# Optimization experiments

Hardware: AMD Instinct MI355X
Metric: run time of the kernel (lower is better)

The kernel has to match this reference:

```python
import jax, jax.numpy as jnp
import numpy as np

SEQ, D, H, DH = 118, 128, 4, 32
NEG = -1e9


def _rope_tables():
    # matches the second (overwriting) computation in __init__: base=10000, dim=128
    ch = jnp.arange(0, D, 2, dtype=jnp.float32)
    inv_freq = 1.0 / (10000.0 ** (ch / D))
    t = jnp.arange(SEQ, dtype=jnp.float32)
    freqs = jnp.outer(t, inv_freq)                      # (118, 64)
    return jnp.cos(freqs).astype(jnp.bfloat16), jnp.sin(freqs).astype(jnp.bfloat16)


def _apply_rope(x, cos, sin):
    # x: (b, 118, 128); cos/sin: (118, 64) bf16 -> promote to f32 in the mul
    d = x.shape[-1] // 2
    x1, x2 = x[..., :d], x[..., d:]
    y1 = x1 * cos + x2 * sin
    y2 = -x1 * sin + x2 * cos
    return jnp.concatenate([y1, y2], axis=-1).astype(x.dtype)


def _layernorm(x, g, b, eps=1e-5):
    mu = jnp.mean(x, -1, keepdims=True)
    var = jnp.mean(jnp.square(x - mu), -1, keepdims=True)
    return (x - mu) * jax.lax.rsqrt(var + eps) * g + b


def _attention_block(x, qkv_w, qkv_b, fc2_w, fc2_b, cos, sin, mask):
    b = x.shape[0]
    qkv = x @ qkv_w.T + qkv_b                           # (b, 118, 384)
    q, k, v = jnp.split(qkv, 3, axis=-1)
    q = _apply_rope(q, cos, sin)
    k = _apply_rope(k, cos, sin)
    # faithful to view(b,118,32,4) + rearrange 'b l d h -> b h l d'
    to_heads = lambda t: jnp.transpose(t.reshape(b, SEQ, DH, H), (0, 3, 1, 2))
    q, k, v = to_heads(q), to_heads(k), to_heads(v)     # (b, 4, 118, 32)
    scores = jnp.einsum('bhqd,bhkd->bhqk', q, k) / jnp.sqrt(jnp.float32(DH))
    scores = jnp.where(mask, scores, NEG)
    attn = jax.nn.softmax(scores, axis=-1)
    y = jnp.einsum('bhqk,bhkd->bhqd', attn, v)          # (b, 4, 118, 32)
    y = jnp.transpose(y, (0, 2, 1, 3)).reshape(b, SEQ, D)
    return jax.nn.silu(y @ fc2_w.T + fc2_b)


def setup_inputs() -> dict:
    key = jax.random.key(0)
    ks = jax.random.split(key, 10)
    s = lambda fan_in: 1.0 / np.sqrt(fan_in)
    inp = {
        'x': jax.random.normal(ks[0], (8192, SEQ), jnp.float32),
        'fc1_w': jax.random.uniform(ks[1], (D, 1), jnp.float32, -1.0, 1.0),
        'fc1_b': jax.random.uniform(ks[2], (D,), jnp.float32, -1.0, 1.0),
        'qkv_w': jax.random.uniform(ks[3], (3 * D, D), jnp.float32, -s(D), s(D)),
        'qkv_b': jax.random.uniform(ks[4], (3 * D,), jnp.float32, -s(D), s(D)),
        'fc2_w': jax.random.uniform(ks[5], (D, D), jnp.float32, -s(D), s(D)),
        'fc2_b': jax.random.uniform(ks[6], (D,), jnp.float32, -s(D), s(D)),
        'fc3_w': jax.random.uniform(ks[7], (1, D), jnp.float32, -s(D), s(D)),
        'fc3_b': jax.random.uniform(ks[8], (1,), jnp.float32, -s(D), s(D)),
        'ln_g': jnp.ones((D,), jnp.float32),
        'ln_b': jnp.zeros((D,), jnp.float32),
    }
    return inp


def reference(x, fc1_w, fc1_b, qkv_w, qkv_b, fc2_w, fc2_b, fc3_w, fc3_b, ln_g, ln_b):
    cos, sin = _rope_tables()
    mask = jnp.tril(jnp.ones((SEQ, SEQ), dtype=bool))
    h = jax.nn.silu(x[..., None] @ fc1_w.T + fc1_b)     # (b, 118, 128)
    x1 = _attention_block(h, qkv_w, qkv_b, fc2_w, fc2_b, cos, sin, mask)
    x2 = x1 + _attention_block(_layernorm(x1, ln_g, ln_b), qkv_w, qkv_b, fc2_w, fc2_b, cos, sin, mask)
    return (x2 @ fc3_w.T + fc3_b).squeeze(-1)           # (b, 118)
```

## Files before the change

### kernel.cpp

```cpp
#include <hip/hip_runtime.h>
#include <hip/hip_bf16.h>

#define SEQ 118
#define YS  136
#define SQS 40
#define SVS 136

typedef __attribute__((ext_vector_type(8))) short short8;
typedef __attribute__((ext_vector_type(4))) float f32x4;

__device__ __forceinline__ f32x4 mfma16(short8 a, short8 b, f32x4 c){
  return __builtin_amdgcn_mfma_f32_16x16x32_bf16(a, b, c, 0, 0, 0);
}
__device__ __forceinline__ float bfr(float x){
  return __bfloat162float(__float2bfloat16(x));
}
__device__ __forceinline__ float rcpf(float x){ return __builtin_amdgcn_rcpf(x); }
__device__ __forceinline__ float fsilu(float z){
  return z * rcpf(1.f + exp2f(-1.442695041f * z));
}
__device__ __forceinline__ float rsum16(float v){
  v += __shfl_xor(v,1); v += __shfl_xor(v,2); v += __shfl_xor(v,4); v += __shfl_xor(v,8);
  return v;
}
__device__ __forceinline__ float rmax16(float v){
  v = fmaxf(v, __shfl_xor(v,1)); v = fmaxf(v, __shfl_xor(v,2));
  v = fmaxf(v, __shfl_xor(v,4)); v = fmaxf(v, __shfl_xor(v,8));
  return v;
}
__device__ __forceinline__ unsigned pack_bf2(float lo, float hi){
  __hip_bfloat162 h2 = __float22bfloat162_rn(float2{lo, hi});
  unsigned u; __builtin_memcpy(&u, &h2, 4);
  return u;
}
__device__ __forceinline__ float bf_lo(unsigned u){
  unsigned v = u << 16; float f; __builtin_memcpy(&f, &v, 4); return f;
}
__device__ __forceinline__ float bf_hi(unsigned u){
  unsigned v = u & 0xffff0000u; float f; __builtin_memcpy(&f, &v, 4); return f;
}

__global__ void prep_kernel(const float* __restrict__ qkv_w,
                            const float* __restrict__ fc2_w,
                            __hip_bfloat16* __restrict__ wbf,
                            unsigned* __restrict__ trig){
  int i = blockIdx.x * 256 + threadIdx.x;
  if (i < 65536){
    int seg = i >> 14;
    int r   = i & 16383;
    int row = r >> 7;
    int k   = r & 127;
    float v;
    if (seg < 3){
      int h = row >> 5, n = row & 31;
      v = qkv_w[(seg*128 + 4*n + h)*128 + k];
    } else {
      int h = k >> 5, rr = k & 31;
      int dh = (rr >> 1) + (rr & 1)*16;
      v = fc2_w[row*128 + h*32 + dh];
    }
    wbf[i] = __float2bfloat16(v);
  } else {
    int ti = i - 65536;
    int h  = ti >> 11;
    int s  = (ti >> 4) & 127;
    int cc = ti & 15;
    float invf = exp2f((float)(4*cc + h) * (-0.20762050593045f));
    float ang  = (float)s * invf;
    trig[ti] = pack_bf2(__cosf(ang), __sinf(ang));
  }
}

template<bool TABLE>
__global__ void
__attribute__((amdgpu_flat_work_group_size(512, 512), amdgpu_waves_per_eu(4, 4)))
fused_kernel(const float* __restrict__ x,
             const float* __restrict__ fc1_w, const float* __restrict__ fc1_b,
             const float* __restrict__ qkv_b,
             const float* __restrict__ fc2_b, const float* __restrict__ fc3_w,
             const float* __restrict__ fc3_b,
             const float* __restrict__ ln_g,  const float* __restrict__ ln_b,
             const __hip_bfloat16* __restrict__ wbf,
             const unsigned* __restrict__ trig,
             float* __restrict__ out)
{
  __shared__ __align__(16) char smem[64864];
  __hip_bfloat16* Ybuf = (__hip_bfloat16*)(smem);
  __hip_bfloat16* sQP  = (__hip_bfloat16*)(smem + 32096);
  __hip_bfloat16* sK   = (__hip_bfloat16*)(smem + 42336);
  __hip_bfloat16* sVt  = (__hip_bfloat16*)(smem + 52576);
  float*          sCb  = (float*)        (smem + 61280);
  float*          sQb  = (float*)        (smem + 63328);

  const __hip_bfloat16* wq  = wbf;
  const __hip_bfloat16* wk  = wbf + 16384;
  const __hip_bfloat16* wvw = wbf + 32768;
  const __hip_bfloat16* w2  = wbf + 49152;

  const int b    = blockIdx.x;
  const int tid  = threadIdx.x;
  const int wv   = tid >> 6;
  const int lane = tid & 63;
  const int c    = lane & 15;
  const int quad = lane >> 4;
  const int arow = wv*16 + c;

  {
    int i = tid;
    if (i < 512){
      float v;
      if      (i < 128) v = fc2_b[i];
      else if (i < 256) v = fc3_w[i-128];
      else if (i < 384) v = ln_g [i-256];
      else              v = ln_b [i-384];
      sCb[i] = v;
    }
    if (i < 384) sQb[i] = qkv_b[i];
  }
  __syncthreads();

  float o1[4];

  #pragma unroll 1
  for (int p = 0; p < 2; ++p){
    short8 afr[4];
    if (p == 0){
      float xs = (arow < SEQ) ? x[b*SEQ + arow] : 0.f;
      #pragma unroll
      for (int k4 = 0; k4 < 4; k4++){
        int d0 = k4*32 + quad*8;
        short8 fr;
        #pragma unroll
        for (int i = 0; i < 8; i++){
          float z = xs * fc1_w[d0+i] + fc1_b[d0+i];
          float v = fsilu(z);
          if (arow >= SEQ) v = 0.f;
          fr[i] = (short)__builtin_bit_cast(unsigned short, __float2bfloat16(v));
        }
        afr[k4] = fr;
      }
    } else {
      #pragma unroll
      for (int k4 = 0; k4 < 4; k4++){
        short8 fr = *(const short8*)(Ybuf + arow*YS + k4*32 + quad*8);
        if (arow >= SEQ) fr = (short8){0,0,0,0,0,0,0,0};
        afr[k4] = fr;
      }
    }

    #pragma unroll 1
    for (int h = 0; h < 4; ++h){
      {
        unsigned tj[4];
        float invf;
        if (TABLE){
          const unsigned* tp = trig + h*2048 + (wv*16 + quad*4)*16 + c;
          tj[0] = tp[0]; tj[1] = tp[16]; tj[2] = tp[32]; tj[3] = tp[48];
        } else {
          invf = exp2f((float)(4*c + h) * (-0.20762050593045f));
        }
        const __hip_bfloat16* wpq = wq + (h*32 + c)*128 + quad*8;
        const __hip_bfloat16* wpk = wk + (h*32 + c)*128 + quad*8;
        f32x4 q0={0,0,0,0}, q1={0,0,0,0}, k0={0,0,0,0}, k1={0,0,0,0};
        #pragma unroll
        for (int k4 = 0; k4 < 4; k4++){
          short8 bq0 = *(const short8*)(wpq + k4*32);
          short8 bq1 = *(const short8*)(wpq + 2048 + k4*32);
          short8 bk0 = *(const short8*)(wpk + k4*32);
          short8 bk1 = *(const short8*)(wpk + 2048 + k4*32);
          q0 = mfma16(afr[k4], bq0, q0);
          q1 = mfma16(afr[k4], bq1, q1);
          k0 = mfma16(afr[k4], bk0, k0);
          k1 = mfma16(afr[k4], bk1, k1);
        }
        const float KSC = 0.25500526963f;
        float bQ0 = sQb[      4*c + h], bQ1 = sQb[ 64 + 4*c + h];
        float bK0 = sQb[128 + 4*c + h], bK1 = sQb[192 + 4*c + h];
        #pragma unroll
        for (int j = 0; j < 4; j++){
          int s = wv*16 + quad*4 + j;
          float cv, sv;
          if (TABLE){
            cv = bf_lo(tj[j]); sv = bf_hi(tj[j]);
          } else {
            float ang = (float)s * invf;
            cv = bfr(__cosf(ang)); sv = bfr(__sinf(ang));
          }
          float cvq = cv*KSC, svq = sv*KSC;
          float xq1 = q0[j] + bQ0, xq2 = q1[j] + bQ1;
          float xk1 = k0[j] + bK0, xk2 = k1[j] + bK1;
          *(unsigned*)(sQP + s*SQS + 2*c) = pack_bf2( xq1*cvq + xq2*svq, -xq1*svq + xq2*cvq);
          *(unsigned*)(sK  + s*SQS + 2*c) = pack_bf2( xk1*cv  + xk2*sv , -xk1*sv  + xk2*cv );
        }
      }
      {
        const __hip_bfloat16* wpv = wvw + (h*32 + c)*128 + quad*8;
        f32x4 v0={0,0,0,0}, v1={0,0,0,0};
        #pragma unroll
        for (int k4 = 0; k4 < 4; k4++){
          short8 b0 = *(const short8*)(wpv + k4*32);
          short8 b1 = *(const short8*)(wpv + 2048 + k4*32);
          v0 = mfma16(afr[k4], b0, v0);
          v1 = mfma16(afr[k4], b1, v1);
        }
        float bV0 = sQb[256 + 4*c + h], bV1 = sQb[320 + 4*c + h];
        int s0 = wv*16 + quad*4;
        *(unsigned*)(sVt + (c   )*SVS + s0    ) = pack_bf2(v0[0]+bV0, v0[1]+bV0);
        *(unsigned*)(sVt + (c   )*SVS + s0 + 2) = pack_bf2(v0[2]+bV0, v0[3]+bV0);
        *(unsigned*)(sVt + (c+16)*SVS + s0    ) = pack_bf2(v1[0]+bV1, v1[1]+bV1);
        *(unsigned*)(sVt + (c+16)*SVS + s0 + 2) = pack_bf2(v1[2]+bV1, v1[3]+bV1);
      }
      __syncthreads();

      short8 aq = *(const short8*)(sQP + arow*SQS + quad*8);
      f32x4 sc[8];
      #pragma unroll
      for (int t = 0; t < 8; t++){
        sc[t] = (f32x4){0.f,0.f,0.f,0.f};
        if (t <= wv){
          short8 bk = *(const short8*)(sK + (t*16 + c)*SQS + quad*8);
          f32x4 z = {0,0,0,0};
          sc[t] = mfma16(aq, bk, z);
        }
      }
      float rnorm[4];
      #pragma unroll
      for (int j = 0; j < 4; j++){
        float mx = -3.0e38f;
        #pragma unroll
        for (int t = 0; t < 8; t++){
          if (t < wv){
            mx = fmaxf(mx, sc[t][j]);
          } else if (t == wv){
            float v = (c <= quad*4 + j) ? sc[t][j] : -1.0e9f;
            sc[t][j] = v;
            mx = fmaxf(mx, v);
          }
        }
        mx = rmax16(mx);
        float sum = 0.f;
        #pragma unroll
        for (int t = 0; t < 8; t++) if (t <= wv){
          float e = exp2f(sc[t][j] - mx); sc[t][j] = e; sum += e;
        }
        sum = rsum16(sum);
        rnorm[j] = rcpf(sum);
      }

      f32x4 y0 = {0,0,0,0}, y1 = {0,0,0,0};
      auto pv_quarter = [&](int qt, f32x4 pa, f32x4 pb){
        int s0 = wv*16 + quad*4;
        #pragma unroll
        for (int j = 0; j < 4; j++){
          sQP[(s0+j)*SQS + c     ] = __float2bfloat16(pa[j]);
          sQP[(s0+j)*SQS + 16 + c] = __float2bfloat16(pb[j]);
        }
        short8 ap  = *(const short8*)(sQP + arow*SQS + quad*8);
        short8 bv0 = *(const short8*)(sVt + (c   )*SVS + qt*32 + quad*8);
        short8 bv1 = *(const short8*)(sVt + (c+16)*SVS + qt*32 + quad*8);
        y0 = mfma16(ap, bv0, y0);
        y1 = mfma16(ap, bv1, y1);
      };
      int qmax = wv >> 1;
      pv_quarter(0, sc[0], sc[1]);
      if (qmax >= 1) pv_quarter(1, sc[2], sc[3]);
      if (qmax >= 2) pv_quarter(2, sc[4], sc[5]);
      if (qmax >= 3) pv_quarter(3, sc[6], sc[7]);
      #pragma unroll
      for (int j = 0; j < 4; j++){ y0[j] *= rnorm[j]; y1[j] *= rnorm[j]; }

      {
        int s0 = wv*16 + quad*4;
        #pragma unroll
        for (int j = 0; j < 4; j++)
          if (s0 + j < SEQ)
            *(unsigned*)(Ybuf + (s0+j)*YS + h*32 + 2*c) = pack_bf2(y0[j], y1[j]);
      }
      __syncthreads();
    }

    short8 ay[4];
    #pragma unroll
    for (int k4 = 0; k4 < 4; k4++)
      ay[k4] = *(const short8*)(Ybuf + arow*YS + k4*32 + quad*8);
    f32x4 xx[8];
    f32x4 S1 = {0,0,0,0}, S2 = {0,0,0,0}, S3 = {0,0,0,0};
    #pragma unroll 1
    for (int t = 0; t < 8; t++){
      f32x4 acc = {0,0,0,0};
      #pragma unroll
      for (int k4 = 0; k4 < 4; k4++){
        short8 bw = *(const short8*)(w2 + (t*16 + c)*128 + k4*32 + quad*8);
        acc = mfma16(ay[k4], bw, acc);
      }
      float bias = sCb[t*16 + c];
      float w3   = sCb[128 + t*16 + c];
      #pragma unroll
      for (int j = 0; j < 4; j++){
        float v = fsilu(acc[j] + bias);
        xx[t][j] = v;
        S1[j] += v; S2[j] += v*v; S3[j] += v*w3;
      }
    }
    #pragma unroll
    for (int j = 0; j < 4; j++){
      float s1 = rsum16(S1[j]), s2 = rsum16(S2[j]), s3 = rsum16(S3[j]);
      int s = wv*16 + quad*4 + j;
      if (p == 0){
        float mu  = s1 * (1.f/128.f);
        float var = fmaxf(s2 * (1.f/128.f) - mu*mu, 0.f);
        float rs  = rsqrtf(var + 1e-5f);
        if (s < SEQ){
          #pragma unroll
          for (int t = 0; t < 8; t++){
            int d = t*16 + c;
            Ybuf[s*YS + d] = __float2bfloat16((xx[t][j] - mu)*rs*sCb[256+d] + sCb[384+d]);
          }
        }
        o1[j] = s3;
      } else {
        if (c == 0 && s < SEQ) out[b*SEQ + s] = o1[j] + s3 + fc3_b[0];
      }
    }
    if (p == 0) __syncthreads();
  }
}

extern "C" void kernel_launch(void* const* d_in, const int* in_sizes, int n_in,
                              void* d_out, int out_size, void* d_ws, size_t ws_size,
                              hipStream_t stream){
  const float* x     = (const float*)d_in[0];
  const float* fc1_w = (const float*)d_in[1];
  const float* fc1_b = (const float*)d_in[2];
  const float* qkv_w = (const float*)d_in[3];
  const float* qkv_b = (const float*)d_in[4];
  const float* fc2_w = (const float*)d_in[5];
  const float* fc2_b = (const float*)d_in[6];
  const float* fc3_w = (const float*)d_in[7];
  const float* fc3_b = (const float*)d_in[8];
  const float* ln_g  = (const float*)d_in[9];
  const float* ln_b  = (const float*)d_in[10];

  __hip_bfloat16* wbf  = (__hip_bfloat16*)d_ws;
  unsigned*       trig = (unsigned*)((char*)d_ws + 131072);
  const bool ut = ws_size >= 131072 + 32768;

  prep_kernel<<<ut ? 288 : 256, 256, 0, stream>>>(qkv_w, fc2_w, wbf, trig);

  const int B = in_sizes[0] / SEQ;
  if (ut)
    fused_kernel<true ><<<B, 512, 0, stream>>>(x, fc1_w, fc1_b, qkv_b, fc2_b, fc3_w,
                                               fc3_b, ln_g, ln_b, wbf, trig, (float*)d_out);
  else
    fused_kernel<false><<<B, 512, 0, stream>>>(x, fc1_w, fc1_b, qkv_b, fc2_b, fc3_w,
                                               fc3_b, ln_g, ln_b, wbf, trig, (float*)d_out);
}
```

Baseline: 2.321 ms.

## Transpose QK^T MFMA and pass softmax probabilities to PV via shuffles

Swaps the MFMA operands for the score computation so each lane holds one query row's scores across the key dimension. Row max and sum then reduce mostly in registers with only two cross-lane shuffles instead of four per row. The bf16-packed probabilities are redistributed into the PV MFMA A-operand layout with lane shuffles, replacing the write to shared memory and read-back. This adds more shuffle instructions and register pressure in exchange for less LDS traffic and fewer reductions.

New measurement: 2.428 ms. 4.6% more time.

```diff
diff --git a/kernel.cpp b/kernel.cpp
--- a/kernel.cpp
+++ b/kernel.cpp
@@ -8,6 +8,7 @@
 
 typedef __attribute__((ext_vector_type(8))) short short8;
 typedef __attribute__((ext_vector_type(4))) float f32x4;
+typedef __attribute__((ext_vector_type(4))) unsigned u32x4;
 
 __device__ __forceinline__ f32x4 mfma16(short8 a, short8 b, f32x4 c){
   return __builtin_amdgcn_mfma_f32_16x16x32_bf16(a, b, c, 0, 0, 0);
@@ -21,11 +22,6 @@
 }
 __device__ __forceinline__ float rsum16(float v){
   v += __shfl_xor(v,1); v += __shfl_xor(v,2); v += __shfl_xor(v,4); v += __shfl_xor(v,8);
-  return v;
-}
-__device__ __forceinline__ float rmax16(float v){
-  v = fmaxf(v, __shfl_xor(v,1)); v = fmaxf(v, __shfl_xor(v,2));
-  v = fmaxf(v, __shfl_xor(v,4)); v = fmaxf(v, __shfl_xor(v,8));
   return v;
 }
 __device__ __forceinline__ unsigned pack_bf2(float lo, float hi){
@@ -220,54 +216,74 @@
         if (t <= wv){
           short8 bk = *(const short8*)(sK + (t*16 + c)*SQS + quad*8);
           f32x4 z = {0,0,0,0};
-          sc[t] = mfma16(aq, bk, z);
-        }
-      }
-      float rnorm[4];
-      #pragma unroll
-      for (int j = 0; j < 4; j++){
-        float mx = -3.0e38f;
-        #pragma unroll
-        for (int t = 0; t < 8; t++){
-          if (t < wv){
-            mx = fmaxf(mx, sc[t][j]);
-          } else if (t == wv){
-            float v = (c <= quad*4 + j) ? sc[t][j] : -1.0e9f;
+          sc[t] = mfma16(bk, aq, z);
+        }
+      }
+      float mx = -3.0e38f;
+      #pragma unroll
+      for (int t = 0; t < 8; t++){
+        if (t < wv){
+          #pragma unroll
+          for (int j = 0; j < 4; j++) mx = fmaxf(mx, sc[t][j]);
+        } else if (t == wv){
+          #pragma unroll
+          for (int j = 0; j < 4; j++){
+            float v = (quad*4 + j <= c) ? sc[t][j] : -1.0e9f;
             sc[t][j] = v;
             mx = fmaxf(mx, v);
           }
         }
-        mx = rmax16(mx);
-        float sum = 0.f;
-        #pragma unroll
-        for (int t = 0; t < 8; t++) if (t <= wv){
-          float e = exp2f(sc[t][j] - mx); sc[t][j] = e; sum += e;
-        }
-        sum = rsum16(sum);
-        rnorm[j] = rcpf(sum);
+      }
+      mx = fmaxf(mx, __shfl_xor(mx, 16));
+      mx = fmaxf(mx, __shfl_xor(mx, 32));
+      float sum = 0.f;
+      #pragma unroll
+      for (int t = 0; t < 8; t++) if (t <= wv){
+        #pragma unroll
+        for (int j = 0; j < 4; j++){
+          float e = exp2f(sc[t][j] - mx);
+          sc[t][j] = e; sum += e;
+        }
+      }
+      sum += __shfl_xor(sum, 16);
+      sum += __shfl_xor(sum, 32);
+      float rnl = rcpf(sum);
+      float rn[4];
+      #pragma unroll
+      for (int j = 0; j < 4; j++) rn[j] = __shfl(rnl, quad*4 + j);
+
+      unsigned pd0[8], pd1[8];
+      #pragma unroll
+      for (int t = 0; t < 8; t++){
+        pd0[t] = pack_bf2(sc[t][0], sc[t][1]);
+        pd1[t] = pack_bf2(sc[t][2], sc[t][3]);
       }
 
       f32x4 y0 = {0,0,0,0}, y1 = {0,0,0,0};
-      auto pv_quarter = [&](int qt, f32x4 pa, f32x4 pb){
-        int s0 = wv*16 + quad*4;
-        #pragma unroll
-        for (int j = 0; j < 4; j++){
-          sQP[(s0+j)*SQS + c     ] = __float2bfloat16(pa[j]);
-          sQP[(s0+j)*SQS + 16 + c] = __float2bfloat16(pb[j]);
-        }
-        short8 ap  = *(const short8*)(sQP + arow*SQS + quad*8);
+      const int srcA = c + ((quad & 1) << 5);
+      const int srcB = srcA + 16;
+      const bool hiq = quad >= 2;
+      auto pv_quarter = [&](int qt){
+        const int te = 2*qt, to = 2*qt + 1;
+        unsigned a0e = __shfl(pd0[te], srcA), a1e = __shfl(pd1[te], srcA);
+        unsigned a2e = __shfl(pd0[te], srcB), a3e = __shfl(pd1[te], srcB);
+        unsigned a0o = __shfl(pd0[to], srcA), a1o = __shfl(pd1[to], srcA);
+        unsigned a2o = __shfl(pd0[to], srcB), a3o = __shfl(pd1[to], srcB);
+        u32x4 aw = { hiq ? a0o : a0e, hiq ? a1o : a1e,
+                     hiq ? a2o : a2e, hiq ? a3o : a3e };
+        short8 ap  = __builtin_bit_cast(short8, aw);
         short8 bv0 = *(const short8*)(sVt + (c   )*SVS + qt*32 + quad*8);
         short8 bv1 = *(const short8*)(sVt + (c+16)*SVS + qt*32 + quad*8);
         y0 = mfma16(ap, bv0, y0);
         y1 = mfma16(ap, bv1, y1);
       };
       int qmax = wv >> 1;
-      pv_quarter(0, sc[0], sc[1]);
-      if (qmax >= 1) pv_quarter(1, sc[2], sc[3]);
-      if (qmax >= 2) pv_quarter(2, sc[4], sc[5]);
-      if (qmax >= 3) pv_quarter(3, sc[6], sc[7]);
-      #pragma unroll
-      for (int j = 0; j < 4; j++){ y0[j] *= rnorm[j]; y1[j] *= rnorm[j]; }
+      pv_quarter(0);
+      if (qmax >= 1) pv_quarter(1);
+      if (qmax >= 2) pv_quarter(2);
+      if (qmax >= 3) pv_quarter(3);
+      #pragma unroll
+      for (int j = 0; j < 4; j++){ y0[j] *= rn[j]; y1[j] *= rn[j]; }
 
       {
         int s0 = wv*16 + quad*4;
```
